# Performance work log

Measured on AMD Instinct MI355X. Metric: run time of the kernel, lower is better.

The kernel has to match this reference:

```python
import jax, jax.numpy as jnp
import numpy as np
from math import sqrt

B, N, D = 16, 4096, 128
M = 64 * 24  # mem_size_per_joint * num_joints


def setup_inputs() -> dict:
    key = jax.random.key(0)
    kx, km = jax.random.split(key)
    x = jax.random.normal(kx, (B, N, D), dtype=jnp.float32)
    mem = jax.random.normal(km, (1, D, M), dtype=jnp.float32)  # N(0,1) init as in torch
    return {"x": x, "mem": mem}


def reference(x, mem):
    # x: (B, N, D); mem: (1, D, M)
    d = x.shape[-1]
    w = mem[0]  # (D, M)
    # logits = bmm(m_key (B,M,D), x_ (B,D,N)) / sqrt(D)  -> (B, M, N)
    logits = jnp.einsum('dm,bnd->bmn', w, x) / sqrt(d)
    # softmax over the memory axis (dim=1 in torch layout)
    attn = jax.nn.softmax(logits, axis=1)  # (B, M, N)
    # x_new = bmm(m (B,D,M), attn) -> (B,D,N); output permuted to (B,N,D)
    out = jnp.einsum('dm,bmn->bnd', w, attn)
    return out
```

## Files before the change

### kernel.cpp

```cpp
#include <hip/hip_runtime.h>
#include <math.h>


#define Bdim 16
#define Ndim 4096
#define Ddim 128
#define Mdim 1536
#define NT 64
#define NTHREADS 256
#define NSESS 12
#define SESS_M 128
#define XPAD 136
#define PPAD 136
#define NFRAG 24576

typedef __attribute__((ext_vector_type(8))) _Float16 f16x8;
typedef __attribute__((ext_vector_type(4))) _Float16 f16x4;
typedef __attribute__((ext_vector_type(4))) float    f32x4;

__global__ void jamb_prep(const float* __restrict__ w,
                          _Float16* __restrict__ wt,
                          _Float16* __restrict__ wd) {
    const int tid = blockIdx.x * 256 + threadIdx.x;
    const float SC = 0.08838834764831843f;
    if (tid < NFRAG) {
        const int f    = tid;
        const int lane = f & 63;
        const int fs   = f >> 6;
        const int ks   = fs & 3;
        const int mt   = fs >> 2;
        const int m    = mt * 16 + (lane & 15);
        const int d0   = ks * 32 + (lane >> 4) * 8;
        f16x8 pk;
        #pragma unroll
        for (int j = 0; j < 8; ++j)
            pk[j] = (_Float16)(w[(size_t)(d0 + j) * Mdim + m] * SC);
        *(f16x8*)&wt[(size_t)f * 8] = pk;
    } else {
        const int f    = tid - NFRAG;
        const int lane = f & 63;
        const int fs   = f >> 6;
        const int km   = fs % 48;
        const int dt   = fs / 48;
        const int d    = dt * 16 + (lane & 15);
        const int m0   = km * 32 + (lane >> 4) * 8;
        const float* src = w + (size_t)d * Mdim + m0;
        const float4 v0 = *(const float4*)src;
        const float4 v1 = *(const float4*)(src + 4);
        f16x8 pk;
        pk[0] = (_Float16)v0.x; pk[1] = (_Float16)v0.y;
        pk[2] = (_Float16)v0.z; pk[3] = (_Float16)v0.w;
        pk[4] = (_Float16)v1.x; pk[5] = (_Float16)v1.y;
        pk[6] = (_Float16)v1.z; pk[7] = (_Float16)v1.w;
        *(f16x8*)&wd[(size_t)f * 8] = pk;
    }
}

__global__ __launch_bounds__(NTHREADS, 4)
void jamb_mfma_kernel(const float* __restrict__ x,
                      const _Float16* __restrict__ wt,
                      const _Float16* __restrict__ wd,
                      float* __restrict__ out) {
    __shared__ __align__(16) _Float16 xs[NT * XPAD];
    __shared__ __align__(16) _Float16 Pbuf[NT * PPAD];
    __shared__ float redsum[4][4][16];

    const int t    = threadIdx.x;
    const int w    = t >> 6;
    const int l    = t & 63;
    const int c16  = l & 15;
    const int quad = l >> 4;

    const int blk   = blockIdx.x;
    const int b     = blk >> 6;
    const int nbase = (blk & 63) * NT;

    {
        const float* xb = x + (size_t)(b * Ndim + nbase) * Ddim;
        #pragma unroll
        for (int i = 0; i < 8; ++i) {
            const int f   = t + i * 256;
            const int row = f >> 5;
            const int c4  = (f & 31) * 4;
            const float4 v = *(const float4*)(xb + row * Ddim + c4);
            f16x4 pk;
            pk[0] = (_Float16)v.x; pk[1] = (_Float16)v.y;
            pk[2] = (_Float16)v.z; pk[3] = (_Float16)v.w;
            *(f16x4*)&xs[row * XPAD + c4] = pk;
        }
    }
    __syncthreads();

    const f16x8* WT = (const f16x8*)wt;
    const f16x8* WD = (const f16x8*)wd;

    float sums[4] = {0.f, 0.f, 0.f, 0.f};
    f32x4 c[2][4];
    #pragma unroll
    for (int i = 0; i < 2; ++i)
        #pragma unroll
        for (int nt = 0; nt < 4; ++nt) c[i][nt] = (f32x4){0.f, 0.f, 0.f, 0.f};

    #pragma unroll 1
    for (int q = 0; q < NSESS; ++q) {
        const int mtb = q * 8 + w * 2;

        f32x4 acc[2][4];
        #pragma unroll
        for (int i = 0; i < 2; ++i)
            #pragma unroll
            for (int nt = 0; nt < 4; ++nt) acc[i][nt] = (f32x4){0.f, 0.f, 0.f, 0.f};

        #pragma unroll
        for (int s = 0; s < 4; ++s) {
            const f16x8 fh0 = WT[((mtb + 0) * 4 + s) * 64 + l];
            const f16x8 fh1 = WT[((mtb + 1) * 4 + s) * 64 + l];
            f16x8 bx[4];
            #pragma unroll
            for (int nt = 0; nt < 4; ++nt)
                bx[nt] = *(const f16x8*)&xs[(nt * 16 + c16) * XPAD + s * 32 + quad * 8];
            #pragma unroll
            for (int nt = 0; nt < 4; ++nt) {
                acc[0][nt] = __builtin_amdgcn_mfma_f32_16x16x32_f16(fh0, bx[nt], acc[0][nt], 0, 0, 0);
                acc[1][nt] = __builtin_amdgcn_mfma_f32_16x16x32_f16(fh1, bx[nt], acc[1][nt], 0, 0, 0);
            }
        }

        #pragma unroll
        for (int i = 0; i < 2; ++i) {
            const int mloc = (w * 2 + i) * 16 + quad * 4;
            #pragma unroll
            for (int nt = 0; nt < 4; ++nt) {
                const float e0 = __expf(acc[i][nt][0]);
                const float e1 = __expf(acc[i][nt][1]);
                const float e2 = __expf(acc[i][nt][2]);
                const float e3 = __expf(acc[i][nt][3]);
                sums[nt] += (e0 + e1) + (e2 + e3);
                f16x4 pk;
                pk[0] = (_Float16)e0; pk[1] = (_Float16)e1;
                pk[2] = (_Float16)e2; pk[3] = (_Float16)e3;
                *(f16x4*)&Pbuf[(nt * 16 + c16) * PPAD + mloc] = pk;
            }
        }
        __syncthreads();

        #pragma unroll
        for (int sk = 0; sk < 4; ++sk) {
            const f16x8 a0 = WD[((2 * w)     * 48 + q * 4 + sk) * 64 + l];
            const f16x8 a1 = WD[((2 * w + 1) * 48 + q * 4 + sk) * 64 + l];
            f16x8 p[4];
            #pragma unroll
            for (int nt = 0; nt < 4; ++nt)
                p[nt] = *(const f16x8*)&Pbuf[(nt * 16 + c16) * PPAD + sk * 32 + quad * 8];
            #pragma unroll
            for (int nt = 0; nt < 4; ++nt) {
                c[0][nt] = __builtin_amdgcn_mfma_f32_16x16x32_f16(a0, p[nt], c[0][nt], 0, 0, 0);
                c[1][nt] = __builtin_amdgcn_mfma_f32_16x16x32_f16(a1, p[nt], c[1][nt], 0, 0, 0);
            }
        }
        __syncthreads();
    }

    #pragma unroll
    for (int nt = 0; nt < 4; ++nt) {
        sums[nt] += __shfl_xor(sums[nt], 16, 64);
        sums[nt] += __shfl_xor(sums[nt], 32, 64);
    }
    if (quad == 0) {
        #pragma unroll
        for (int nt = 0; nt < 4; ++nt) redsum[w][nt][c16] = sums[nt];
    }
    __syncthreads();

    float inv[4];
    #pragma unroll
    for (int nt = 0; nt < 4; ++nt)
        inv[nt] = 1.f / ((redsum[0][nt][c16] + redsum[1][nt][c16]) +
                         (redsum[2][nt][c16] + redsum[3][nt][c16]));

    #pragma unroll
    for (int dt2 = 0; dt2 < 2; ++dt2) {
        #pragma unroll
        for (int nt = 0; nt < 4; ++nt) {
            float* op = out + (size_t)(b * Ndim + nbase + nt * 16 + c16) * Ddim
                           + (2 * w + dt2) * 16 + quad * 4;
            float4 o;
            o.x = c[dt2][nt][0] * inv[nt];
            o.y = c[dt2][nt][1] * inv[nt];
            o.z = c[dt2][nt][2] * inv[nt];
            o.w = c[dt2][nt][3] * inv[nt];
            *(float4*)op = o;
        }
    }
}

extern "C" void kernel_launch(void* const* d_in, const int* in_sizes, int n_in,
                              void* d_out, int out_size, void* d_ws, size_t ws_size,
                              hipStream_t stream) {
    const float* x = (const float*)d_in[0];
    const float* w = (const float*)d_in[1];
    float* out = (float*)d_out;
    (void)in_sizes; (void)n_in; (void)out_size; (void)ws_size;

    _Float16* wt = (_Float16*)d_ws;
    _Float16* wd = wt + Ddim * Mdim;

    jamb_prep<<<dim3((2 * NFRAG) / 256), dim3(256), 0, stream>>>(w, wt, wd);
    jamb_mfma_kernel<<<dim3((Bdim * Ndim) / NT), dim3(NTHREADS), 0, stream>>>(x, wt, wd, out);
}
```

Baseline: 134.9 us.

## Software-pipeline logits and output GEMMs with double-buffered P tile

Splits the memory axis into 24 sessions of 64 instead of 12 of 128 and double-buffers the softmax P tile in shared memory. The second GEMM for session q-1 now runs in the same iteration as the first GEMM for session q, which halves the block barriers per session from two to one. WT fragments are prefetched into registers one session ahead. This is meant to overlap exp and LDS work with MFMA and cut sync stalls, at the cost of more live registers, which could lower occupancy under the launch bound of 4.

```diff
diff --git a/kernel.cpp b/kernel.cpp
--- a/kernel.cpp
+++ b/kernel.cpp
@@ -8,10 +8,9 @@
 #define Mdim 1536
 #define NT 64
 #define NTHREADS 256
-#define NSESS 12
-#define SESS_M 128
+#define NSESS 24
 #define XPAD 136
-#define PPAD 136
+#define PPAD 72
 #define NFRAG 24576
 
 typedef __attribute__((ext_vector_type(8))) _Float16 f16x8;
@@ -62,7 +61,7 @@
                       const _Float16* __restrict__ wd,
                       float* __restrict__ out) {
     __shared__ __align__(16) _Float16 xs[NT * XPAD];
-    __shared__ __align__(16) _Float16 Pbuf[NT * PPAD];
+    __shared__ __align__(16) _Float16 Pbuf[2][NT * PPAD];
     __shared__ float redsum[4][4][16];
 
     const int t    = threadIdx.x;
@@ -101,64 +100,87 @@
         #pragma unroll
         for (int nt = 0; nt < 4; ++nt) c[i][nt] = (f32x4){0.f, 0.f, 0.f, 0.f};
 
+    f16x8 wtf[4];
+    #pragma unroll
+    for (int s = 0; s < 4; ++s) wtf[s] = WT[((0 * 4 + w) * 4 + s) * 64 + l];
+
     #pragma unroll 1
     for (int q = 0; q < NSESS; ++q) {
-        const int mtb = q * 8 + w * 2;
-
-        f32x4 acc[2][4];
-        #pragma unroll
-        for (int i = 0; i < 2; ++i)
-            #pragma unroll
-            for (int nt = 0; nt < 4; ++nt) acc[i][nt] = (f32x4){0.f, 0.f, 0.f, 0.f};
-
+        const int bq = q & 1;
+
+        f16x8 wtn[4];
+        {
+            const int mtn = (q + 1 < NSESS ? (q + 1) * 4 + w : q * 4 + w);
+            #pragma unroll
+            for (int s = 0; s < 4; ++s) wtn[s] = WT[(mtn * 4 + s) * 64 + l];
+        }
+        f16x8 wdv[2][2];
+        if (q) {
+            #pragma unroll
+            for (int dt2 = 0; dt2 < 2; ++dt2)
+                #pragma unroll
+                for (int ks = 0; ks < 2; ++ks)
+                    wdv[dt2][ks] = WD[((2 * w + dt2) * 48 + (q - 1) * 2 + ks) * 64 + l];
+        }
+
+        f32x4 a1[4];
+        #pragma unroll
+        for (int nt = 0; nt < 4; ++nt) a1[nt] = (f32x4){0.f, 0.f, 0.f, 0.f};
         #pragma unroll
         for (int s = 0; s < 4; ++s) {
-            const f16x8 fh0 = WT[((mtb + 0) * 4 + s) * 64 + l];
-            const f16x8 fh1 = WT[((mtb + 1) * 4 + s) * 64 + l];
-            f16x8 bx[4];
-            #pragma unroll
-            for (int nt = 0; nt < 4; ++nt)
-                bx[nt] = *(const f16x8*)&xs[(nt * 16 + c16) * XPAD + s * 32 + quad * 8];
             #pragma unroll
             for (int nt = 0; nt < 4; ++nt) {
-                acc[0][nt] = __builtin_amdgcn_mfma_f32_16x16x32_f16(fh0, bx[nt], acc[0][nt], 0, 0, 0);
-                acc[1][nt] = __builtin_amdgcn_mfma_f32_16x16x32_f16(fh1, bx[nt], acc[1][nt], 0, 0, 0);
+                const f16x8 bx = *(const f16x8*)&xs[(nt * 16 + c16) * XPAD + s * 32 + quad * 8];
+                a1[nt] = __builtin_amdgcn_mfma_f32_16x16x32_f16(wtf[s], bx, a1[nt], 0, 0, 0);
             }
         }
 
         #pragma unroll
-        for (int i = 0; i < 2; ++i) {
-            const int mloc = (w * 2 + i) * 16 + quad * 4;
+        for (int nt = 0; nt < 4; ++nt) {
+            const float e0 = __expf(a1[nt][0]);
+            const float e1 = __expf(a1[nt][1]);
+            const float e2 = __expf(a1[nt][2]);
+            const float e3 = __expf(a1[nt][3]);
+            sums[nt] += (e0 + e1) + (e2 + e3);
+            f16x4 pk;
+            pk[0] = (_Float16)e0; pk[1] = (_Float16)e1;
+            pk[2] = (_Float16)e2; pk[3] = (_Float16)e3;
+            *(f16x4*)&Pbuf[bq][(nt * 16 + c16) * PPAD + w * 16 + quad * 4] = pk;
+        }
+
+        if (q) {
+            #pragma unroll
+            for (int ks = 0; ks < 2; ++ks) {
+                #pragma unroll
+                for (int nt = 0; nt < 4; ++nt) {
+                    const f16x8 p = *(const f16x8*)&Pbuf[1 - bq][(nt * 16 + c16) * PPAD + ks * 32 + quad * 8];
+                    c[0][nt] = __builtin_amdgcn_mfma_f32_16x16x32_f16(wdv[0][ks], p, c[0][nt], 0, 0, 0);
+                    c[1][nt] = __builtin_amdgcn_mfma_f32_16x16x32_f16(wdv[1][ks], p, c[1][nt], 0, 0, 0);
+                }
+            }
+        }
+
+        __syncthreads();
+        #pragma unroll
+        for (int s = 0; s < 4; ++s) wtf[s] = wtn[s];
+    }
+
+    {
+        f16x8 wdv[2][2];
+        #pragma unroll
+        for (int dt2 = 0; dt2 < 2; ++dt2)
+            #pragma unroll
+            for (int ks = 0; ks < 2; ++ks)
+                wdv[dt2][ks] = WD[((2 * w + dt2) * 48 + (NSESS - 1) * 2 + ks) * 64 + l];
+        #pragma unroll
+        for (int ks = 0; ks < 2; ++ks) {
             #pragma unroll
             for (int nt = 0; nt < 4; ++nt) {
-                const float e0 = __expf(acc[i][nt][0]);
-                const float e1 = __expf(acc[i][nt][1]);
-                const float e2 = __expf(acc[i][nt][2]);
-                const float e3 = __expf(acc[i][nt][3]);
-                sums[nt] += (e0 + e1) + (e2 + e3);
-                f16x4 pk;
-                pk[0] = (_Float16)e0; pk[1] = (_Float16)e1;
-                pk[2] = (_Float16)e2; pk[3] = (_Float16)e3;
-                *(f16x4*)&Pbuf[(nt * 16 + c16) * PPAD + mloc] = pk;
+                const f16x8 p = *(const f16x8*)&Pbuf[1][(nt * 16 + c16) * PPAD + ks * 32 + quad * 8];
+                c[0][nt] = __builtin_amdgcn_mfma_f32_16x16x32_f16(wdv[0][ks], p, c[0][nt], 0, 0, 0);
+                c[1][nt] = __builtin_amdgcn_mfma_f32_16x16x32_f16(wdv[1][ks], p, c[1][nt], 0, 0, 0);
             }
         }
-        __syncthreads();
-
-        #pragma unroll
-        for (int sk = 0; sk < 4; ++sk) {
-            const f16x8 a0 = WD[((2 * w)     * 48 + q * 4 + sk) * 64 + l];
-            const f16x8 a1 = WD[((2 * w + 1) * 48 + q * 4 + sk) * 64 + l];
-            f16x8 p[4];
-            #pragma unroll
-            for (int nt = 0; nt < 4; ++nt)
-                p[nt] = *(const f16x8*)&Pbuf[(nt * 16 + c16) * PPAD + sk * 32 + quad * 8];
-            #pragma unroll
-            for (int nt = 0; nt < 4; ++nt) {
-                c[0][nt] = __builtin_amdgcn_mfma_f32_16x16x32_f16(a0, p[nt], c[0][nt], 0, 0, 0);
-                c[1][nt] = __builtin_amdgcn_mfma_f32_16x16x32_f16(a1, p[nt], c[1][nt], 0, 0, 0);
-            }
-        }
-        __syncthreads();
     }
 
     #pragma unroll
```

Result: slower. 138.2 us (+2.5%).

## Switch to 32x32x16 MFMA tiles with XOR-swizzled LDS layout

Applied to the files above, without the earlier changes.

Replaces the 16x16x32 f16 MFMA tiling with 32x32x16 MFMAs in both the logits and output GEMMs, and re-lays out the prepacked weight fragments to match. The padded LDS buffers for x and the softmax probabilities become unpadded and XOR-swizzled to avoid bank conflicts. The intent is to cut the instruction count and the LDS/global fragment loads per FLOP, since each weight fragment now feeds a larger tile. The cost is larger accumulator register footprint, which may hurt occupancy under the 4-wave launch bound, and the swizzle arithmetic must match between writes and reads.

```diff
diff --git a/kernel.cpp b/kernel.cpp
--- a/kernel.cpp
+++ b/kernel.cpp
@@ -9,14 +9,11 @@
 #define NT 64
 #define NTHREADS 256
 #define NSESS 12
-#define SESS_M 128
-#define XPAD 136
-#define PPAD 136
 #define NFRAG 24576
 
-typedef __attribute__((ext_vector_type(8))) _Float16 f16x8;
-typedef __attribute__((ext_vector_type(4))) _Float16 f16x4;
-typedef __attribute__((ext_vector_type(4))) float    f32x4;
+typedef __attribute__((ext_vector_type(8)))  _Float16 f16x8;
+typedef __attribute__((ext_vector_type(4)))  _Float16 f16x4;
+typedef __attribute__((ext_vector_type(16))) float    f32x16;
 
 __global__ void jamb_prep(const float* __restrict__ w,
                           _Float16* __restrict__ wt,
@@ -25,12 +22,12 @@
     const float SC = 0.08838834764831843f;
     if (tid < NFRAG) {
         const int f    = tid;
-        const int lane = f & 63;
+        const int l    = f & 63;
         const int fs   = f >> 6;
-        const int ks   = fs & 3;
-        const int mt   = fs >> 2;
-        const int m    = mt * 16 + (lane & 15);
-        const int d0   = ks * 32 + (lane >> 4) * 8;
+        const int ks   = fs & 7;
+        const int mt   = fs >> 3;
+        const int m    = mt * 32 + (l & 31);
+        const int d0   = ks * 16 + (l >> 5) * 8;
         f16x8 pk;
         #pragma unroll
         for (int j = 0; j < 8; ++j)
@@ -38,12 +35,12 @@
         *(f16x8*)&wt[(size_t)f * 8] = pk;
     } else {
         const int f    = tid - NFRAG;
-        const int lane = f & 63;
+        const int l    = f & 63;
         const int fs   = f >> 6;
-        const int km   = fs % 48;
-        const int dt   = fs / 48;
-        const int d    = dt * 16 + (lane & 15);
-        const int m0   = km * 32 + (lane >> 4) * 8;
+        const int km   = fs % 96;
+        const int dt   = fs / 96;
+        const int d    = dt * 32 + (l & 31);
+        const int m0   = km * 16 + (l >> 5) * 8;
         const float* src = w + (size_t)d * Mdim + m0;
         const float4 v0 = *(const float4*)src;
         const float4 v1 = *(const float4*)(src + 4);
@@ -61,15 +58,15 @@
                       const _Float16* __restrict__ wt,
                       const _Float16* __restrict__ wd,
                       float* __restrict__ out) {
-    __shared__ __align__(16) _Float16 xs[NT * XPAD];
-    __shared__ __align__(16) _Float16 Pbuf[NT * PPAD];
-    __shared__ float redsum[4][4][16];
+    __shared__ __align__(16) _Float16 xs[NT * 128];
+    __shared__ __align__(16) _Float16 Pbuf[NT * 128];
+    __shared__ float redsum[4][NT];
 
     const int t    = threadIdx.x;
     const int w    = t >> 6;
     const int l    = t & 63;
-    const int c16  = l & 15;
-    const int quad = l >> 4;
+    const int c32  = l & 31;
+    const int half = l >> 5;
 
     const int blk   = blockIdx.x;
     const int b     = blk >> 6;
@@ -86,7 +83,8 @@
             f16x4 pk;
             pk[0] = (_Float16)v.x; pk[1] = (_Float16)v.y;
             pk[2] = (_Float16)v.z; pk[3] = (_Float16)v.w;
-            *(f16x4*)&xs[row * XPAD + c4] = pk;
+            const int g = ((c4 >> 3) ^ (row & 15)) << 3;
+            *(f16x4*)&xs[row * 128 + g + (c4 & 7)] = pk;
         }
     }
     __syncthreads();
@@ -94,101 +92,97 @@
     const f16x8* WT = (const f16x8*)wt;
     const f16x8* WD = (const f16x8*)wd;
 
-    float sums[4] = {0.f, 0.f, 0.f, 0.f};
-    f32x4 c[2][4];
+    float sums[2] = {0.f, 0.f};
+    f32x16 c0 = {0.f}, c1 = {0.f};
     #pragma unroll
-    for (int i = 0; i < 2; ++i)
-        #pragma unroll
-        for (int nt = 0; nt < 4; ++nt) c[i][nt] = (f32x4){0.f, 0.f, 0.f, 0.f};
+    for (int r = 0; r < 16; ++r) { c0[r] = 0.f; c1[r] = 0.f; }
+
+    const int swz = c32 & 15;
 
     #pragma unroll 1
     for (int q = 0; q < NSESS; ++q) {
-        const int mtb = q * 8 + w * 2;
-
-        f32x4 acc[2][4];
-        #pragma unroll
-        for (int i = 0; i < 2; ++i)
-            #pragma unroll
-            for (int nt = 0; nt < 4; ++nt) acc[i][nt] = (f32x4){0.f, 0.f, 0.f, 0.f};
-
-        #pragma unroll
-        for (int s = 0; s < 4; ++s) {
-            const f16x8 fh0 = WT[((mtb + 0) * 4 + s) * 64 + l];
-            const f16x8 fh1 = WT[((mtb + 1) * 4 + s) * 64 + l];
-            f16x8 bx[4];
-            #pragma unroll
-            for (int nt = 0; nt < 4; ++nt)
-                bx[nt] = *(const f16x8*)&xs[(nt * 16 + c16) * XPAD + s * 32 + quad * 8];
-            #pragma unroll
-            for (int nt = 0; nt < 4; ++nt) {
-                acc[0][nt] = __builtin_amdgcn_mfma_f32_16x16x32_f16(fh0, bx[nt], acc[0][nt], 0, 0, 0);
-                acc[1][nt] = __builtin_amdgcn_mfma_f32_16x16x32_f16(fh1, bx[nt], acc[1][nt], 0, 0, 0);
-            }
-        }
-
-        #pragma unroll
-        for (int i = 0; i < 2; ++i) {
-            const int mloc = (w * 2 + i) * 16 + quad * 4;
-            #pragma unroll
-            for (int nt = 0; nt < 4; ++nt) {
-                const float e0 = __expf(acc[i][nt][0]);
-                const float e1 = __expf(acc[i][nt][1]);
-                const float e2 = __expf(acc[i][nt][2]);
-                const float e3 = __expf(acc[i][nt][3]);
-                sums[nt] += (e0 + e1) + (e2 + e3);
+        f32x16 a0 = {0.f}, a1 = {0.f};
+        #pragma unroll
+        for (int r = 0; r < 16; ++r) { a0[r] = 0.f; a1[r] = 0.f; }
+        #pragma unroll
+        for (int ks = 0; ks < 8; ++ks) {
+            const f16x8 af = WT[((q * 4 + w) * 8 + ks) * 64 + l];
+            const int g = (((ks * 2 + half) ^ swz) << 3);
+            const f16x8 b0 = *(const f16x8*)&xs[c32 * 128 + g];
+            const f16x8 b1 = *(const f16x8*)&xs[(32 + c32) * 128 + g];
+            a0 = __builtin_amdgcn_mfma_f32_32x32x16_f16(af, b0, a0, 0, 0, 0);
+            a1 = __builtin_amdgcn_mfma_f32_32x32x16_f16(af, b1, a1, 0, 0, 0);
+        }
+
+        #pragma unroll
+        for (int rq = 0; rq < 4; ++rq) {
+            const int gq = ((w * 4 + rq) ^ swz) << 3;
+            const int oq = half * 4;
+            {
+                const float e0 = __expf(a0[rq * 4 + 0]);
+                const float e1 = __expf(a0[rq * 4 + 1]);
+                const float e2 = __expf(a0[rq * 4 + 2]);
+                const float e3 = __expf(a0[rq * 4 + 3]);
+                sums[0] += (e0 + e1) + (e2 + e3);
                 f16x4 pk;
                 pk[0] = (_Float16)e0; pk[1] = (_Float16)e1;
                 pk[2] = (_Float16)e2; pk[3] = (_Float16)e3;
-                *(f16x4*)&Pbuf[(nt * 16 + c16) * PPAD + mloc] = pk;
+                *(f16x4*)&Pbuf[c32 * 128 + gq + oq] = pk;
             }
+            {
+                const float e0 = __expf(a1[rq * 4 + 0]);
+                const float e1 = __expf(a1[rq * 4 + 1]);
+                const float e2 = __expf(a1[rq * 4 + 2]);
+                const float e3 = __expf(a1[rq * 4 + 3]);
+                sums[1] += (e0 + e1) + (e2 + e3);
+                f16x4 pk;
+                pk[0] = (_Float16)e0; pk[1] = (_Float16)e1;
+                pk[2] = (_Float16)e2; pk[3] = (_Float16)e3;
+                *(f16x4*)&Pbuf[(32 + c32) * 128 + gq + oq] = pk;
+            }
         }
         __syncthreads();
 
         #pragma unroll
-        for (int sk = 0; sk < 4; ++sk) {
-            const f16x8 a0 = WD[((2 * w)     * 48 + q * 4 + sk) * 64 + l];
-            const f16x8 a1 = WD[((2 * w + 1) * 48 + q * 4 + sk) * 64 + l];
-            f16x8 p[4];
-            #pragma unroll
-            for (int nt = 0; nt < 4; ++nt)
-                p[nt] = *(const f16x8*)&Pbuf[(nt * 16 + c16) * PPAD + sk * 32 + quad * 8];
-            #pragma unroll
-            for (int nt = 0; nt < 4; ++nt) {
-                c[0][nt] = __builtin_amdgcn_mfma_f32_16x16x32_f16(a0, p[nt], c[0][nt], 0, 0, 0);
-                c[1][nt] = __builtin_amdgcn_mfma_f32_16x16x32_f16(a1, p[nt], c[1][nt], 0, 0, 0);
-            }
+        for (int km = 0; km < 8; ++km) {
+            const f16x8 wdf = WD[(w * 96 + q * 8 + km) * 64 + l];
+            const int g = (((km * 2 + half) ^ swz) << 3);
+            const f16x8 p0 = *(const f16x8*)&Pbuf[c32 * 128 + g];
+            const f16x8 p1 = *(const f16x8*)&Pbuf[(32 + c32) * 128 + g];
+            c0 = __builtin_amdgcn_mfma_f32_32x32x16_f16(wdf, p0, c0, 0, 0, 0);
+            c1 = __builtin_amdgcn_mfma_f32_32x32x16_f16(wdf, p1, c1, 0, 0, 0);
         }
         __syncthreads();
     }
 
+    sums[0] += __shfl_xor(sums[0], 32, 64);
+    sums[1] += __shfl_xor(sums[1], 32, 64);
+    if (half == 0) {
+        redsum[w][c32]      = sums[0];
+        redsum[w][32 + c32] = sums[1];
+    }
+    __syncthreads();
+
+    const float inv0 = 1.f / (redsum[0][c32] + redsum[1][c32] +
+                              redsum[2][c32] + redsum[3][c32]);
+    const float inv1 = 1.f / (redsum[0][32 + c32] + redsum[1][32 + c32] +
+                              redsum[2][32 + c32] + redsum[3][32 + c32]);
+
     #pragma unroll
-    for (int nt = 0; nt < 4; ++nt) {
-        sums[nt] += __shfl_xor(sums[nt], 16, 64);
-        sums[nt] += __shfl_xor(sums[nt], 32, 64);
-    }
-    if (quad == 0) {
-        #pragma unroll
-        for (int nt = 0; nt < 4; ++nt) redsum[w][nt][c16] = sums[nt];
-    }
-    __syncthreads();
-
-    float inv[4];
-    #pragma unroll
-    for (int nt = 0; nt < 4; ++nt)
-        inv[nt] = 1.f / ((redsum[0][nt][c16] + redsum[1][nt][c16]) +
-                         (redsum[2][nt][c16] + redsum[3][nt][c16]));
-
-    #pragma unroll
-    for (int dt2 = 0; dt2 < 2; ++dt2) {
-        #pragma unroll
-        for (int nt = 0; nt < 4; ++nt) {
-            float* op = out + (size_t)(b * Ndim + nbase + nt * 16 + c16) * Ddim
-                           + (2 * w + dt2) * 16 + quad * 4;
+    for (int rq = 0; rq < 4; ++rq) {
+        const int d = w * 32 + rq * 8 + half * 4;
+        {
+            float* op = out + (size_t)(b * Ndim + nbase + c32) * Ddim + d;
             float4 o;
-            o.x = c[dt2][nt][0] * inv[nt];
-            o.y = c[dt2][nt][1] * inv[nt];
-            o.z = c[dt2][nt][2] * inv[nt];
-            o.w = c[dt2][nt][3] * inv[nt];
+            o.x = c0[rq * 4 + 0] * inv0; o.y = c0[rq * 4 + 1] * inv0;
+            o.z = c0[rq * 4 + 2] * inv0; o.w = c0[rq * 4 + 3] * inv0;
+            *(float4*)op = o;
+        }
+        {
+            float* op = out + (size_t)(b * Ndim + nbase + 32 + c32) * Ddim + d;
+            float4 o;
+            o.x = c1[rq * 4 + 0] * inv1; o.y = c1[rq * 4 + 1] * inv1;
+            o.z = c1[rq * 4 + 2] * inv1; o.w = c1[rq * 4 + 3] * inv1;
             *(float4*)op = o;
         }
     }
```

New measurement: 140.3 us. 1.04x slower.
